# Performance work log

Measured on AMD Instinct MI355X. Metric: run time of the kernel, lower is better.

The kernel has to match this reference:

```python
import jax, jax.numpy as jnp
import numpy as np

EPS = 1e-7  # tf.keras.backend.epsilon()
NUM_HEADS = 8


def setup_inputs() -> dict:
    key = jax.random.key(0)
    ks = jax.random.split(key, 7)
    B, H, W, C = 4, 128, 128, 512
    glorot = (2.0 / (C + C)) ** 0.5
    x = jax.random.normal(ks[0], (B, H, W, C), dtype=jnp.float32)
    wq = jax.random.normal(ks[1], (C, C), dtype=jnp.float32) * glorot
    bq = jnp.zeros((C,), dtype=jnp.float32)
    wk = jax.random.normal(ks[2], (C, C), dtype=jnp.float32) * glorot
    bk = jnp.zeros((C,), dtype=jnp.float32)
    wv = jax.random.normal(ks[3], (C, C), dtype=jnp.float32) * glorot
    bv = jnp.zeros((C,), dtype=jnp.float32)
    return {"x": x, "wq": wq, "bq": bq, "wk": wk, "bk": bk, "wv": wv, "bv": bv}


def _axial_attention(query, key, value, num_heads):
    B, H, W, C = value.shape
    d = query.shape[-1] // num_heads
    q5 = query.reshape(B, H, W, num_heads, d)
    k5 = key.reshape(B, H, W, num_heads, d)
    # column (vertical) attention: scores over H, per column w -> [B, nh, W, H, H]
    v_att = jnp.einsum("bhwnd,bgwnd->bnwhg", q5, k5)
    # row (horizontal) attention: scores over W, per row h -> [B, nh, H, W, W]
    u_att = jnp.einsum("bhwnd,bhvnd->bnhwv", q5, k5)
    # faithful clip-before-softmax chain from the original module
    v_att = jnp.clip(v_att, -1.0 + EPS, 1.0 - EPS)
    u_att = jnp.clip(u_att, -1.0 + EPS, 1.0 - EPS)
    scale = jnp.sqrt(jnp.asarray(d, dtype=v_att.dtype))
    v_att = v_att / scale
    u_att = u_att / scale
    # safed_softmax: softmax in fp32 (inputs already fp32 here)
    v_att = jax.nn.softmax(v_att.astype(jnp.float32), axis=-1).astype(query.dtype)
    u_att = jax.nn.softmax(u_att.astype(jnp.float32), axis=-1).astype(query.dtype)
    v_att = jnp.where(jnp.isnan(v_att), EPS, v_att)
    u_att = jnp.where(jnp.isnan(u_att), EPS, u_att)
    v_att = jnp.clip(v_att, EPS, 1.0 - EPS)
    u_att = jnp.clip(u_att, EPS, 1.0 - EPS)
    # value: [B, nh, W, H, d]
    val5 = value.reshape(B, H, W, num_heads, d)
    xv = jnp.einsum("bnwhg,bnwgd->bnhwd", v_att, val5.transpose(0, 3, 2, 1, 4))
    xu = jnp.einsum("bnhwv,bnhvd->bnhwd", u_att, xv)
    # transpose (0,2,3,4,1): head index becomes last -> channels ordered [d, nh]
    out = xu.transpose(0, 2, 3, 4, 1).reshape(B, H, W, d * num_heads)
    return out


def reference(x, wq, bq, wk, bk, wv, bv):
    # 1x1 convs == per-pixel dense projections
    query = jnp.einsum("bhwc,cf->bhwf", x, wq) + bq
    key = jnp.einsum("bhwc,cf->bhwf", x, wk) + bk
    value = jnp.einsum("bhwc,cf->bhwf", x, wv) + bv
    return _axial_attention(query, key, value, NUM_HEADS)
```

## Files before the change

### kernel.cpp

```cpp
#include <hip/hip_runtime.h>

typedef unsigned short ush;
typedef __attribute__((ext_vector_type(8))) __bf16 bf16x8;
typedef __attribute__((ext_vector_type(4))) float f32x4;

#define NE 33554432L

__device__ __forceinline__ float b2f(ush u) {
  return __uint_as_float(((unsigned int)u) << 16);
}
__device__ __forceinline__ ush f2b(float f) {
  unsigned int x = __float_as_uint(f);
  x += 0x7fffu + ((x >> 16) & 1u);
  return (ush)(x >> 16);
}
__device__ __forceinline__ bf16x8 bc8(int4 v) { return __builtin_bit_cast(bf16x8, v); }

__device__ __forceinline__ void gload16(const ush* g, ush* l) {
  __builtin_amdgcn_global_load_lds(
      (const __attribute__((address_space(1))) void*)g,
      (__attribute__((address_space(3))) void*)l, 16, 0, 0);
}

__global__ __launch_bounds__(256)
void detect_dtype(const ush* __restrict__ x, int* __restrict__ flag) {
  __shared__ int red[256];
  const int t = threadIdx.x;
  int cnt = 0;
  for (int i = t; i < 16384; i += 256) {
    const int e = (x[i] >> 7) & 0xFF;
    cnt += (e == 0 || (e >= 100 && e <= 142)) ? 1 : 0;
  }
  red[t] = cnt;
  __syncthreads();
  for (int s = 128; s > 0; s >>= 1) {
    if (t < s) red[t] += red[t + s];
    __syncthreads();
  }
  if (t == 0) flag[0] = (red[0] >= 13107) ? 1 : 0;
}

__global__ __launch_bounds__(256)
void pack_x(const void* __restrict__ xin, ush* __restrict__ xb,
            const int* __restrict__ flag) {
  const long i0 = ((long)blockIdx.x * 256 + threadIdx.x) * 8;
  if (*flag) {
    *(int4*)&xb[i0] = *(const int4*)&((const ush*)xin)[i0];
  } else {
    const float* xf = (const float*)xin;
    const float4 a = *(const float4*)&xf[i0];
    const float4 b = *(const float4*)&xf[i0 + 4];
    union { ush u[8]; int4 v; } r;
    r.u[0] = f2b(a.x); r.u[1] = f2b(a.y); r.u[2] = f2b(a.z); r.u[3] = f2b(a.w);
    r.u[4] = f2b(b.x); r.u[5] = f2b(b.y); r.u[6] = f2b(b.z); r.u[7] = f2b(b.w);
    *(int4*)&xb[i0] = r.v;
  }
}

__global__ __launch_bounds__(256)
void pack_w(const void* __restrict__ w0, const void* __restrict__ w1,
            const void* __restrict__ w2, ush* __restrict__ wTb,
            const int* __restrict__ flag) {
  __shared__ ush tile[32][33];
  const void* w = (blockIdx.z == 0) ? w0 : ((blockIdx.z == 1) ? w1 : w2);
  ush* wT = wTb + (long)blockIdx.z * 262144;
  const int bx = blockIdx.x * 32, by = blockIdx.y * 32;
  const int tx = threadIdx.x & 31, ty = threadIdx.x >> 5;
  const int f = *flag;
#pragma unroll
  for (int j = 0; j < 32; j += 8) {
    const int k = by + ty + j, n = bx + tx;
    tile[ty + j][tx] = f ? ((const ush*)w)[k * 512 + n]
                         : f2b(((const float*)w)[k * 512 + n]);
  }
  __syncthreads();
#pragma unroll
  for (int j = 0; j < 32; j += 8)
    wT[(bx + ty + j) * 512 + by + tx] = tile[tx][ty + j];
}

__global__ void pack_bias(const void* __restrict__ b0, const void* __restrict__ b1,
                          const void* __restrict__ b2, float* __restrict__ biasf,
                          const int* __restrict__ flag) {
  const void* b = (blockIdx.x == 0) ? b0 : ((blockIdx.x == 1) ? b1 : b2);
  const int n = threadIdx.x;
  const float v = (*flag) ? b2f(((const ush*)b)[n]) : ((const float*)b)[n];
  biasf[blockIdx.x * 512 + n] = v;
}

__global__ __launch_bounds__(256)
void proj_gemm(const ush* __restrict__ xb, const ush* __restrict__ wTb,
               const float* __restrict__ biasf, ush* __restrict__ qkv) {
  __shared__ ush As[2][4096];
  __shared__ ush Bs[2][4096];

  const int z = blockIdx.z;
  const ush* wt = wTb + (long)z * 262144;
  const float* bias = biasf + z * 512;
  ush* out = qkv + (long)z * NE;

  const int t = threadIdx.x;
  const int lane = t & 63;
  const int wvid = t >> 6;
  const int wm = wvid & 1, wn = wvid >> 1;
  const int col = lane & 15, quad = lane >> 4;

  const long m0 = (long)blockIdx.y * 128;
  const int n0 = blockIdx.x * 128;

  const int r_in_g = lane >> 2;
  const int swz = (((lane & 3) ^ ((r_in_g >> 1) & 3)) * 8);
  const int g0 = wvid * 2, g1 = g0 + 1;
  const ush* gA0 = xb + (m0 + g0 * 16 + r_in_g) * 512 + swz;
  const ush* gA1 = xb + (m0 + g1 * 16 + r_in_g) * 512 + swz;
  const ush* gB0 = wt + (long)(n0 + g0 * 16 + r_in_g) * 512 + swz;
  const ush* gB1 = wt + (long)(n0 + g1 * 16 + r_in_g) * 512 + swz;

  const int kswz = ((quad ^ ((col >> 1) & 3)) * 8);
  int aofs[4], bofs4[4];
#pragma unroll
  for (int i = 0; i < 4; i++) aofs[i] = (wm * 64 + i * 16 + col) * 32 + kswz;
#pragma unroll
  for (int j = 0; j < 4; j++) bofs4[j] = (wn * 64 + j * 16 + col) * 32 + kswz;

  const f32x4 z4 = {0.f, 0.f, 0.f, 0.f};
  f32x4 acc[4][4];
#pragma unroll
  for (int i = 0; i < 4; i++)
#pragma unroll
    for (int j = 0; j < 4; j++) acc[i][j] = z4;

  gload16(gA0, &As[0][g0 * 512]);
  gload16(gA1, &As[0][g1 * 512]);
  gload16(gB0, &Bs[0][g0 * 512]);
  gload16(gB1, &Bs[0][g1 * 512]);
  __syncthreads();

  int cur = 0;
  for (int k0 = 0; k0 < 512; k0 += 32) {
    const int nk = k0 + 32;
    if (nk < 512) {
      const int nb = cur ^ 1;
      gload16(gA0 + nk, &As[nb][g0 * 512]);
      gload16(gA1 + nk, &As[nb][g1 * 512]);
      gload16(gB0 + nk, &Bs[nb][g0 * 512]);
      gload16(gB1 + nk, &Bs[nb][g1 * 512]);
    }
    bf16x8 a[4], b[4];
#pragma unroll
    for (int i = 0; i < 4; i++) a[i] = bc8(*(const int4*)&As[cur][aofs[i]]);
#pragma unroll
    for (int j = 0; j < 4; j++) b[j] = bc8(*(const int4*)&Bs[cur][bofs4[j]]);
#pragma unroll
    for (int i = 0; i < 4; i++)
#pragma unroll
      for (int j = 0; j < 4; j++)
        acc[i][j] = __builtin_amdgcn_mfma_f32_16x16x32_bf16(a[i], b[j], acc[i][j], 0, 0, 0);
    __syncthreads();
    cur ^= 1;
  }

#pragma unroll
  for (int j = 0; j < 4; j++) {
    const int n = n0 + wn * 64 + j * 16 + col;
    const float bb = bias[n];
#pragma unroll
    for (int i = 0; i < 4; i++) {
      const long row0 = m0 + wm * 64 + i * 16 + quad * 4;
#pragma unroll
      for (int r = 0; r < 4; r++)
        out[(row0 + r) * 512 + n] = f2b(acc[i][j][r] + bb);
    }
  }
}

#define QS_STRIDE 72
#define VT_STRIDE 136
#define P_STRIDE  136
#define OS_STRIDE 72

__device__ __forceinline__ int vt_idx(int d, int g) {
  return d * VT_STRIDE + ((((g >> 3) ^ ((d >> 3) & 7)) << 3) | (g & 7));
}

template<int PASS>
__global__ __launch_bounds__(256, 3)
void axial_attn_mfma(const ush* __restrict__ Qb, const ush* __restrict__ Kb,
                     ush* __restrict__ Vb, float* __restrict__ xuf,
                     const int bofs) {
  __shared__ ush smem[27136];
  ush* Qs = smem;
  ush* Ks = smem + 9216;
  ush* Vt = smem + 18432;
  ush* P  = smem;

  const int b = blockIdx.z + bofs, n = blockIdx.y, pp = blockIdx.x;
  long base; int stride;
  if (PASS == 1) { base = ((long)b * 16384 + pp) * 512 + n * 64; stride = 65536; }
  else           { base = ((long)(b * 128 + pp) * 128) * 512 + n * 64; stride = 512; }

  const int t = threadIdx.x;
#pragma unroll
  for (int it = 0; it < 4; it++) {
    const int c = t + it * 256;
    const int row = c >> 3, c8 = c & 7;
    const long g = base + (long)row * stride + c8 * 8;
    int4 q = *(const int4*)(Qb + g);
    int4 k = *(const int4*)(Kb + g);
    int4 v = *(const int4*)(Vb + g);
    *(int4*)&Qs[row * QS_STRIDE + c8 * 8] = q;
    *(int4*)&Ks[row * QS_STRIDE + c8 * 8] = k;
    union { int4 i4; ush u[8]; } vu; vu.i4 = v;
#pragma unroll
    for (int dd = 0; dd < 8; dd++)
      Vt[vt_idx(c8 * 8 + dd, row)] = vu.u[dd];
  }
  __syncthreads();

  const int lane = t & 63, wv = t >> 6;
  const int col = lane & 15, quad = lane >> 4;
  const int m0 = wv * 32;
  const f32x4 z4 = {0.f, 0.f, 0.f, 0.f};

  f32x4 sacc[2][8];
#pragma unroll
  for (int i = 0; i < 2; i++)
#pragma unroll
    for (int j = 0; j < 8; j++) sacc[i][j] = z4;
  __builtin_amdgcn_s_setprio(1);
#pragma unroll
  for (int k0 = 0; k0 < 64; k0 += 32) {
    bf16x8 a[2], kb[8];
#pragma unroll
    for (int i = 0; i < 2; i++)
      a[i] = bc8(*(const int4*)&Qs[(m0 + i * 16 + col) * QS_STRIDE + k0 + quad * 8]);
#pragma unroll
    for (int j = 0; j < 8; j++)
      kb[j] = bc8(*(const int4*)&Ks[(j * 16 + col) * QS_STRIDE + k0 + quad * 8]);
#pragma unroll
    for (int i = 0; i < 2; i++)
#pragma unroll
      for (int j = 0; j < 8; j++)
        sacc[i][j] = __builtin_amdgcn_mfma_f32_16x16x32_bf16(a[i], kb[j], sacc[i][j], 0, 0, 0);
  }
  __builtin_amdgcn_s_setprio(0);

  const float CLIP = 1.0f - 1e-7f;
  float e[2][8][4], inv[2][4];
#pragma unroll
  for (int i = 0; i < 2; i++)
#pragma unroll
    for (int r = 0; r < 4; r++) {
      float part = 0.f;
#pragma unroll
      for (int j = 0; j < 8; j++) {
        float s = sacc[i][j][r];
        s = fminf(fmaxf(s, -CLIP), CLIP) * 0.125f;
        const float ee = __expf(s);
        e[i][j][r] = ee;
        part += ee;
      }
      part += __shfl_xor(part, 1);
      part += __shfl_xor(part, 2);
      part += __shfl_xor(part, 4);
      part += __shfl_xor(part, 8);
      inv[i][r] = 1.0f / part;
    }
  __syncthreads();

#pragma unroll
  for (int i = 0; i < 2; i++)
#pragma unroll
    for (int r = 0; r < 4; r++) {
      const int row = m0 + i * 16 + quad * 4 + r;
#pragma unroll
      for (int j = 0; j < 8; j++) {
        const float pv = fminf(fmaxf(e[i][j][r] * inv[i][r], 1e-7f), CLIP);
        P[row * P_STRIDE + j * 16 + col] = f2b(pv);
      }
    }
  __syncthreads();

  f32x4 oacc[2][4];
#pragma unroll
  for (int i = 0; i < 2; i++)
#pragma unroll
    for (int j = 0; j < 4; j++) oacc[i][j] = z4;
  __builtin_amdgcn_s_setprio(1);
#pragma unroll
  for (int k0 = 0; k0 < 128; k0 += 32) {
    bf16x8 a[2], vb[4];
#pragma unroll
    for (int i = 0; i < 2; i++)
      a[i] = bc8(*(const int4*)&P[(m0 + i * 16 + col) * P_STRIDE + k0 + quad * 8]);
#pragma unroll
    for (int j = 0; j < 4; j++)
      vb[j] = bc8(*(const int4*)&Vt[vt_idx(j * 16 + col, k0 + quad * 8)]);
#pragma unroll
    for (int i = 0; i < 2; i++)
#pragma unroll
      for (int j = 0; j < 4; j++)
        oacc[i][j] = __builtin_amdgcn_mfma_f32_16x16x32_bf16(a[i], vb[j], oacc[i][j], 0, 0, 0);
  }
  __builtin_amdgcn_s_setprio(0);

  if (PASS == 1) {
    __syncthreads();
    ush* Os = smem;
#pragma unroll
    for (int i = 0; i < 2; i++)
#pragma unroll
      for (int r = 0; r < 4; r++) {
        const int row = m0 + i * 16 + quad * 4 + r;
#pragma unroll
        for (int j = 0; j < 4; j++)
          Os[row * OS_STRIDE + j * 16 + col] = f2b(oacc[i][j][r]);
      }
    __syncthreads();
#pragma unroll
    for (int it = 0; it < 4; it++) {
      const int g2 = t + it * 256;
      const int row = g2 >> 3, c8 = g2 & 7;
      *(int4*)&Vb[base + (long)row * stride + c8 * 8] =
          *(const int4*)&Os[row * OS_STRIDE + c8 * 8];
    }
  } else {
    const long xbase = (((long)(blockIdx.z * 8 + n) * 128 + pp) * 128) * 64;
#pragma unroll
    for (int i = 0; i < 2; i++)
#pragma unroll
      for (int r = 0; r < 4; r++) {
        const int row = m0 + i * 16 + quad * 4 + r;
#pragma unroll
        for (int j = 0; j < 4; j++)
          xuf[xbase + (long)row * 64 + j * 16 + col] = oacc[i][j][r];
      }
  }
}

__global__ __launch_bounds__(256)
void out_interleave(const float* __restrict__ xu, void* __restrict__ outp,
                    const int* __restrict__ flagp, const int bofs) {
  __shared__ float lds[8192];
  const int bz = blockIdx.z, h = blockIdx.y, w0 = blockIdx.x * 16;
  const int t = threadIdx.x;
#pragma unroll
  for (int n = 0; n < 8; n++) {
    const float* src = xu + ((((long)(bz * 8 + n)) * 128 + h) * 128 + w0) * 64;
    const int e = t * 4, w = e >> 6, d = e & 63;
    const float4 v = *(const float4*)&src[e];
    const int dr = (d + n * 8) & 63;
    *(float4*)&lds[(n * 16 + w) * 64 + dr] = v;
  }
  __syncthreads();
  const int flg = *flagp;
  const long obase = (((long)(bz + bofs) * 128 + h) * 128 + w0) * 512;
  const int tc = t & 127, c0 = tc * 4;
  const int d = c0 >> 3, n0 = c0 & 7;
#pragma unroll
  for (int ro = 0; ro < 8; ro++) {
    const int w = (t >> 7) * 8 + ro;
    float r[4];
#pragma unroll
    for (int k = 0; k < 4; k++) {
      const int n = n0 + k;
      r[k] = lds[(n * 16 + w) * 64 + ((d + n * 8) & 63)];
    }
    const long oi = obase + (long)w * 512 + c0;
    if (flg) {
      union { ush u[4]; int2 v; } o;
      o.u[0] = f2b(r[0]); o.u[1] = f2b(r[1]);
      o.u[2] = f2b(r[2]); o.u[3] = f2b(r[3]);
      *(int2*)&((ush*)outp)[oi] = o.v;
    } else {
      float4 o; o.x = r[0]; o.y = r[1]; o.z = r[2]; o.w = r[3];
      *(float4*)&((float*)outp)[oi] = o;
    }
  }
}

extern "C" void kernel_launch(void* const* d_in, const int* in_sizes, int n_in,
                              void* d_out, int out_size, void* d_ws, size_t ws_size,
                              hipStream_t stream) {
  const void* x  = d_in[0];
  const void* wq = d_in[1];
  const void* bq = d_in[2];
  const void* wk = d_in[3];
  const void* bk = d_in[4];
  const void* wv = d_in[5];
  const void* bv = d_in[6];

  char* ws = (char*)d_ws;
  int*   flag  = (int*)ws;
  float* biasf = (float*)(ws + 256);
  ush*   wTb   = (ush*)(ws + 8192);
  ush*   xb    = (ush*)(ws + 8192 + 1572864);
  float* xuf   = (float*)(ws + 8192 + 1572864);
  ush*   qkv   = (ush*)(ws + 8192 + 1572864 + 67108864);

  dim3 blk(256);
  detect_dtype<<<1, blk, 0, stream>>>((const ush*)x, flag);
  pack_bias<<<3, 512, 0, stream>>>(bq, bk, bv, biasf, flag);
  pack_w<<<dim3(16, 16, 3), blk, 0, stream>>>(wq, wk, wv, wTb, flag);
  pack_x<<<16384, blk, 0, stream>>>(x, xb, flag);

  ush* Q = qkv;
  ush* K = Q + NE;
  ush* V = K + NE;
  proj_gemm<<<dim3(4, 512, 3), blk, 0, stream>>>(xb, wTb, biasf, Q);
  axial_attn_mfma<1><<<dim3(128, 8, 4), blk, 0, stream>>>(Q, K, V, nullptr, 0);
  for (int half = 0; half < 2; half++) {
    axial_attn_mfma<2><<<dim3(128, 8, 2), blk, 0, stream>>>(Q, K, V, xuf, half * 2);
    out_interleave<<<dim3(8, 128, 2), blk, 0, stream>>>(xuf, d_out, flag, half * 2);
  }
}
```

Baseline: 590.0 us.

## Use 8 waves per attention block and swizzle projection GEMM block order

The axial attention kernel now runs 512 threads per block, with each of its 8 waves handling 16 query rows instead of 32. The aim is more latency hiding and lower per-wave register pressure, at the cost of reloading the K and V fragments in more waves. The projection GEMM also remaps its linear block index with an interleaved swizzle, which changes which tiles run together and may improve cache locality across the three weight matrices. Shared-memory use per attention block is unchanged, so occupancy may end up limited by LDS.

```diff
diff --git a/kernel.cpp b/kernel.cpp
--- a/kernel.cpp
+++ b/kernel.cpp
@@ -94,7 +94,12 @@
   __shared__ ush As[2][4096];
   __shared__ ush Bs[2][4096];
 
-  const int z = blockIdx.z;
+  const int lin = blockIdx.x + (blockIdx.y << 2) + (blockIdx.z << 11);
+  const int swz = ((lin & 7) * 768) + (lin >> 3);
+  const int z   = swz >> 11;
+  const int rem = swz & 2047;
+  const int by  = rem >> 2, bx = rem & 3;
+
   const ush* wt = wTb + (long)z * 262144;
   const float* bias = biasf + z * 512;
   ush* out = qkv + (long)z * NE;
@@ -105,16 +110,16 @@
   const int wm = wvid & 1, wn = wvid >> 1;
   const int col = lane & 15, quad = lane >> 4;
 
-  const long m0 = (long)blockIdx.y * 128;
-  const int n0 = blockIdx.x * 128;
+  const long m0 = (long)by * 128;
+  const int n0 = bx * 128;
 
   const int r_in_g = lane >> 2;
-  const int swz = (((lane & 3) ^ ((r_in_g >> 1) & 3)) * 8);
+  const int swzk = (((lane & 3) ^ ((r_in_g >> 1) & 3)) * 8);
   const int g0 = wvid * 2, g1 = g0 + 1;
-  const ush* gA0 = xb + (m0 + g0 * 16 + r_in_g) * 512 + swz;
-  const ush* gA1 = xb + (m0 + g1 * 16 + r_in_g) * 512 + swz;
-  const ush* gB0 = wt + (long)(n0 + g0 * 16 + r_in_g) * 512 + swz;
-  const ush* gB1 = wt + (long)(n0 + g1 * 16 + r_in_g) * 512 + swz;
+  const ush* gA0 = xb + (m0 + g0 * 16 + r_in_g) * 512 + swzk;
+  const ush* gA1 = xb + (m0 + g1 * 16 + r_in_g) * 512 + swzk;
+  const ush* gB0 = wt + (long)(n0 + g0 * 16 + r_in_g) * 512 + swzk;
+  const ush* gB1 = wt + (long)(n0 + g1 * 16 + r_in_g) * 512 + swzk;
 
   const int kswz = ((quad ^ ((col >> 1) & 3)) * 8);
   int aofs[4], bofs4[4];
@@ -184,7 +189,7 @@
 }
 
 template<int PASS>
-__global__ __launch_bounds__(256, 3)
+__global__ __launch_bounds__(512, 4)
 void axial_attn_mfma(const ush* __restrict__ Qb, const ush* __restrict__ Kb,
                      ush* __restrict__ Vb, float* __restrict__ xuf,
                      const int bofs) {
@@ -201,8 +206,8 @@
 
   const int t = threadIdx.x;
 #pragma unroll
-  for (int it = 0; it < 4; it++) {
-    const int c = t + it * 256;
+  for (int it = 0; it < 2; it++) {
+    const int c = t + it * 512;
     const int row = c >> 3, c8 = c & 7;
     const long g = base + (long)row * stride + c8 * 8;
     int4 q = *(const int4*)(Qb + g);
@@ -219,88 +224,72 @@
 
   const int lane = t & 63, wv = t >> 6;
   const int col = lane & 15, quad = lane >> 4;
-  const int m0 = wv * 32;
+  const int m0 = wv * 16;
   const f32x4 z4 = {0.f, 0.f, 0.f, 0.f};
 
-  f32x4 sacc[2][8];
-#pragma unroll
-  for (int i = 0; i < 2; i++)
-#pragma unroll
-    for (int j = 0; j < 8; j++) sacc[i][j] = z4;
+  f32x4 sacc[8];
+#pragma unroll
+  for (int j = 0; j < 8; j++) sacc[j] = z4;
   __builtin_amdgcn_s_setprio(1);
 #pragma unroll
   for (int k0 = 0; k0 < 64; k0 += 32) {
-    bf16x8 a[2], kb[8];
-#pragma unroll
-    for (int i = 0; i < 2; i++)
-      a[i] = bc8(*(const int4*)&Qs[(m0 + i * 16 + col) * QS_STRIDE + k0 + quad * 8]);
+    bf16x8 a, kb[8];
+    a = bc8(*(const int4*)&Qs[(m0 + col) * QS_STRIDE + k0 + quad * 8]);
 #pragma unroll
     for (int j = 0; j < 8; j++)
       kb[j] = bc8(*(const int4*)&Ks[(j * 16 + col) * QS_STRIDE + k0 + quad * 8]);
 #pragma unroll
-    for (int i = 0; i < 2; i++)
-#pragma unroll
-      for (int j = 0; j < 8; j++)
-        sacc[i][j] = __builtin_amdgcn_mfma_f32_16x16x32_bf16(a[i], kb[j], sacc[i][j], 0, 0, 0);
+    for (int j = 0; j < 8; j++)
+      sacc[j] = __builtin_amdgcn_mfma_f32_16x16x32_bf16(a, kb[j], sacc[j], 0, 0, 0);
   }
   __builtin_amdgcn_s_setprio(0);
 
   const float CLIP = 1.0f - 1e-7f;
-  float e[2][8][4], inv[2][4];
-#pragma unroll
-  for (int i = 0; i < 2; i++)
-#pragma unroll
-    for (int r = 0; r < 4; r++) {
-      float part = 0.f;
-#pragma unroll
-      for (int j = 0; j < 8; j++) {
-        float s = sacc[i][j][r];
-        s = fminf(fmaxf(s, -CLIP), CLIP) * 0.125f;
-        const float ee = __expf(s);
-        e[i][j][r] = ee;
-        part += ee;
-      }
-      part += __shfl_xor(part, 1);
-      part += __shfl_xor(part, 2);
-      part += __shfl_xor(part, 4);
-      part += __shfl_xor(part, 8);
-      inv[i][r] = 1.0f / part;
-    }
-  __syncthreads();
-
-#pragma unroll
-  for (int i = 0; i < 2; i++)
-#pragma unroll
-    for (int r = 0; r < 4; r++) {
-      const int row = m0 + i * 16 + quad * 4 + r;
-#pragma unroll
-      for (int j = 0; j < 8; j++) {
-        const float pv = fminf(fmaxf(e[i][j][r] * inv[i][r], 1e-7f), CLIP);
-        P[row * P_STRIDE + j * 16 + col] = f2b(pv);
-      }
-    }
-  __syncthreads();
-
-  f32x4 oacc[2][4];
-#pragma unroll
-  for (int i = 0; i < 2; i++)
-#pragma unroll
-    for (int j = 0; j < 4; j++) oacc[i][j] = z4;
+  float e[8][4], inv[4];
+#pragma unroll
+  for (int r = 0; r < 4; r++) {
+    float part = 0.f;
+#pragma unroll
+    for (int j = 0; j < 8; j++) {
+      float s = sacc[j][r];
+      s = fminf(fmaxf(s, -CLIP), CLIP) * 0.125f;
+      const float ee = __expf(s);
+      e[j][r] = ee;
+      part += ee;
+    }
+    part += __shfl_xor(part, 1);
+    part += __shfl_xor(part, 2);
+    part += __shfl_xor(part, 4);
+    part += __shfl_xor(part, 8);
+    inv[r] = 1.0f / part;
+  }
+  __syncthreads();
+
+#pragma unroll
+  for (int r = 0; r < 4; r++) {
+    const int row = m0 + quad * 4 + r;
+#pragma unroll
+    for (int j = 0; j < 8; j++) {
+      const float pv = fminf(fmaxf(e[j][r] * inv[r], 1e-7f), CLIP);
+      P[row * P_STRIDE + j * 16 + col] = f2b(pv);
+    }
+  }
+  __syncthreads();
+
+  f32x4 oacc[4];
+#pragma unroll
+  for (int j = 0; j < 4; j++) oacc[j] = z4;
   __builtin_amdgcn_s_setprio(1);
 #pragma unroll
   for (int k0 = 0; k0 < 128; k0 += 32) {
-    bf16x8 a[2], vb[4];
-#pragma unroll
-    for (int i = 0; i < 2; i++)
-      a[i] = bc8(*(const int4*)&P[(m0 + i * 16 + col) * P_STRIDE + k0 + quad * 8]);
+    bf16x8 a, vb[4];
+    a = bc8(*(const int4*)&P[(m0 + col) * P_STRIDE + k0 + quad * 8]);
 #pragma unroll
     for (int j = 0; j < 4; j++)
       vb[j] = bc8(*(const int4*)&Vt[vt_idx(j * 16 + col, k0 + quad * 8)]);
 #pragma unroll
-    for (int i = 0; i < 2; i++)
-#pragma unroll
-      for (int j = 0; j < 4; j++)
-        oacc[i][j] = __builtin_amdgcn_mfma_f32_16x16x32_bf16(a[i], vb[j], oacc[i][j], 0, 0, 0);
+    for (int j = 0; j < 4; j++)
+      oacc[j] = __builtin_amdgcn_mfma_f32_16x16x32_bf16(a, vb[j], oacc[j], 0, 0, 0);
   }
   __builtin_amdgcn_s_setprio(0);
 
@@ -308,18 +297,16 @@
     __syncthreads();
     ush* Os = smem;
 #pragma unroll
-    for (int i = 0; i < 2; i++)
-#pragma unroll
-      for (int r = 0; r < 4; r++) {
-        const int row = m0 + i * 16 + quad * 4 + r;
-#pragma unroll
-        for (int j = 0; j < 4; j++)
-          Os[row * OS_STRIDE + j * 16 + col] = f2b(oacc[i][j][r]);
-      }
+    for (int r = 0; r < 4; r++) {
+      const int row = m0 + quad * 4 + r;
+#pragma unroll
+      for (int j = 0; j < 4; j++)
+        Os[row * OS_STRIDE + j * 16 + col] = f2b(oacc[j][r]);
+    }
     __syncthreads();
 #pragma unroll
-    for (int it = 0; it < 4; it++) {
-      const int g2 = t + it * 256;
+    for (int it = 0; it < 2; it++) {
+      const int g2 = t + it * 512;
       const int row = g2 >> 3, c8 = g2 & 7;
       *(int4*)&Vb[base + (long)row * stride + c8 * 8] =
           *(const int4*)&Os[row * OS_STRIDE + c8 * 8];
@@ -327,14 +314,12 @@
   } else {
     const long xbase = (((long)(blockIdx.z * 8 + n) * 128 + pp) * 128) * 64;
 #pragma unroll
-    for (int i = 0; i < 2; i++)
-#pragma unroll
-      for (int r = 0; r < 4; r++) {
-        const int row = m0 + i * 16 + quad * 4 + r;
-#pragma unroll
-        for (int j = 0; j < 4; j++)
-          xuf[xbase + (long)row * 64 + j * 16 + col] = oacc[i][j][r];
-      }
+    for (int r = 0; r < 4; r++) {
+      const int row = m0 + quad * 4 + r;
+#pragma unroll
+      for (int j = 0; j < 4; j++)
+        xuf[xbase + (long)row * 64 + j * 16 + col] = oacc[j][r];
+    }
   }
 }
 
@@ -408,9 +393,9 @@
   ush* K = Q + NE;
   ush* V = K + NE;
   proj_gemm<<<dim3(4, 512, 3), blk, 0, stream>>>(xb, wTb, biasf, Q);
-  axial_attn_mfma<1><<<dim3(128, 8, 4), blk, 0, stream>>>(Q, K, V, nullptr, 0);
+  axial_attn_mfma<1><<<dim3(128, 8, 4), dim3(512), 0, stream>>>(Q, K, V, nullptr, 0);
   for (int half = 0; half < 2; half++) {
-    axial_attn_mfma<2><<<dim3(128, 8, 2), blk, 0, stream>>>(Q, K, V, xuf, half * 2);
+    axial_attn_mfma<2><<<dim3(128, 8, 2), dim3(512), 0, stream>>>(Q, K, V, xuf, half * 2);
     out_interleave<<<dim3(8, 128, 2), blk, 0, stream>>>(xuf, d_out, flag, half * 2);
   }
 }
```

Result: faster. 546.7 us (-7.3%).
